# Kernel optimization log

Measured on AMD Instinct MI355X. Metric: run time of the kernel, lower is better.

The kernel has to match this reference:

```python
import jax, jax.numpy as jnp
import numpy as np

SL, BS, D = 2048, 2, 1024
H, DH = 16, 64  # num_heads, nhid

def setup_inputs() -> dict:
    key = jax.random.key(0)
    ks = jax.random.split(key, 8)
    inv = 1.0 / np.sqrt(D)
    return {
        "query": jax.random.normal(ks[0], (SL, BS, D), jnp.float32),
        "keys": jax.random.normal(ks[1], (SL, BS, D), jnp.float32),
        "values": jax.random.normal(ks[2], (SL, BS, D), jnp.float32),
        "mask": jnp.ones((1, 1, SL, SL), jnp.int32),
        "Wq": jax.random.normal(ks[3], (H * DH, D), jnp.float32) * inv,
        "Wk": jax.random.normal(ks[4], (H * DH, D), jnp.float32) * inv,
        "Wv": jax.random.normal(ks[5], (H * DH, D), jnp.float32) * inv,
        "Wo": jax.random.normal(ks[6], (D, H * DH), jnp.float32) * inv,
    }

def reference(query, keys, values, mask, Wq, Wk, Wv, Wo):
    slq, bs, _ = query.shape
    sl = keys.shape[0]
    # nn.Linear(bias=False): x @ W.T ; then view to (s, b, H, DH)
    q = (query @ Wq.T).reshape(slq, bs, H, DH)   # sbhd
    k = (keys @ Wk.T).reshape(sl, bs, H, DH)
    v = (values @ Wv.T).reshape(sl, bs, H, DH)
    # NOTE: original forward never applies self.scale -> unscaled scores.
    scores = jnp.einsum('qbhd,kbhd->bhqk', q, k)
    scores = jnp.where(mask == 0, jnp.float32(-1e20), scores)
    weights = jax.nn.softmax(scores, axis=-1)
    attn = jnp.einsum('bhqk,kbhd->qbhd', weights, v).reshape(slq, bs, H * DH)
    return attn @ Wo.T  # [slq, bs, out_dim]
```

## Files before the change

### kernel.cpp

```cpp
#include <hip/hip_runtime.h>


typedef __attribute__((ext_vector_type(4))) float  f32x4;
typedef __attribute__((ext_vector_type(8))) __bf16 bf16x8;
typedef __attribute__((ext_vector_type(4))) __bf16 bf16x4;

#define SLEN 2048
#define BSZ  2
#define DMODEL 1024
#define NHEAD 16
#define DHEAD 64
#define D2 (2 * DMODEL)

__device__ __forceinline__ void async16(void* lds, const void* g) {
    __builtin_amdgcn_global_load_lds(
        (const __attribute__((address_space(1))) unsigned int*)g,
        (__attribute__((address_space(3))) unsigned int*)lds, 16, 0, 0);
}

__device__ __forceinline__ f32x4 mfma16(bf16x8 a, bf16x8 b, f32x4 c) {
    return __builtin_amdgcn_mfma_f32_16x16x32_bf16(a, b, c, 0, 0, 0);
}

struct CvtArgs {
    const float* src[7];
    __bf16* dst[7];
    int n4[7];
    float scale[7];
    const int* mask;
    unsigned int* flag;
    int maskn4;
};
__global__ void cvt_all(CvtArgs a) {
    const int t = blockIdx.y;
    const int stride = gridDim.x * blockDim.x;
    if (t == 7) {
        bool ok = true;
        for (int i = blockIdx.x * blockDim.x + threadIdx.x; i < a.maskn4; i += stride) {
            int4 v = ((const int4*)a.mask)[i];
            ok = ok && v.x && v.y && v.z && v.w;
        }
        if (!ok) atomicAnd(a.flag, 0u);
        return;
    }
    const float* __restrict__ src = a.src[t];
    __bf16* __restrict__ dst = a.dst[t];
    const int n4 = a.n4[t];
    const float sc = a.scale[t];
    for (int i = blockIdx.x * blockDim.x + threadIdx.x; i < n4; i += stride) {
        float4 v = ((const float4*)src)[i];
        bf16x4 o;
        o[0] = (__bf16)(v.x * sc); o[1] = (__bf16)(v.y * sc);
        o[2] = (__bf16)(v.z * sc); o[3] = (__bf16)(v.w * sc);
        ((bf16x4*)dst)[i] = o;
    }
}

__global__ __launch_bounds__(256, 3) void gemm_qkv(const __bf16* __restrict__ Xq,
                                                   const __bf16* __restrict__ Xk,
                                                   const __bf16* __restrict__ Xv,
                                                   const __bf16* __restrict__ W,
                                                   __bf16* __restrict__ QK,
                                                   __bf16* __restrict__ VT) {
    __shared__ __bf16 At[128 * 64];
    __shared__ __bf16 Bt[128 * 64];
    const int tid = threadIdx.x;
    const int lane = tid & 63, wv = tid >> 6;
    const int l15 = lane & 15, l4 = lane >> 4;
    const int wr = wv >> 1, wc = wv & 1;
    const int srow = lane >> 3;
    const int sbyte = (((lane & 7) ^ srow) << 4);
    const int bm = blockIdx.x, bn = blockIdx.y;
    const __bf16* A = (bn < 8) ? Xq : (bn < 16) ? Xk : Xv;
    const char* Ab = (const char*)(A + (size_t)bm * 128 * DMODEL);
    const char* Bb = (const char*)(W + (size_t)bn * 128 * DMODEL);

    f32x4 acc[4][4];
#pragma unroll
    for (int m = 0; m < 4; m++)
#pragma unroll
        for (int n = 0; n < 4; n++)
#pragma unroll
            for (int r = 0; r < 4; r++) acc[m][n][r] = 0.0f;

    for (int k0 = 0; k0 < DMODEL; k0 += 64) {
        __syncthreads();
#pragma unroll
        for (int i = 0; i < 8; i++) {
            int c = wv * 8 + i;
            if (c < 16) {
                int row = c * 8 + srow;
                async16(&At[c * 512], Ab + ((size_t)row * DMODEL + k0) * 2 + sbyte);
            } else {
                int row = (c - 16) * 8 + srow;
                async16(&Bt[(c - 16) * 512], Bb + ((size_t)row * DMODEL + k0) * 2 + sbyte);
            }
        }
        __syncthreads();

#pragma unroll
        for (int kk = 0; kk < 2; kk++) {
            bf16x8 af[4], bfr[4];
#pragma unroll
            for (int m = 0; m < 4; m++) {
                int row = wr * 64 + m * 16 + l15;
                int col = (kk * 32 + l4 * 8) ^ ((row & 7) << 3);
                af[m] = *(const bf16x8*)&At[row * 64 + col];
            }
#pragma unroll
            for (int n = 0; n < 4; n++) {
                int row = wc * 64 + n * 16 + l15;
                int col = (kk * 32 + l4 * 8) ^ ((row & 7) << 3);
                bfr[n] = *(const bf16x8*)&Bt[row * 64 + col];
            }
#pragma unroll
            for (int m = 0; m < 4; m++)
#pragma unroll
                for (int n = 0; n < 4; n++)
                    acc[m][n] = mfma16(af[m], bfr[n], acc[m][n]);
        }
    }

    if (bn < 16) {
#pragma unroll
        for (int m = 0; m < 4; m++)
#pragma unroll
            for (int n = 0; n < 4; n++)
#pragma unroll
                for (int r = 0; r < 4; r++) {
                    size_t row = (size_t)bm * 128 + wr * 64 + m * 16 + l4 * 4 + r;
                    size_t col = (size_t)bn * 128 + wc * 64 + n * 16 + l15;
                    QK[row * D2 + col] = (__bf16)acc[m][n][r];
                }
    } else {
#pragma unroll
        for (int m = 0; m < 4; m++)
#pragma unroll
            for (int n = 0; n < 4; n++)
#pragma unroll
                for (int r = 0; r < 4; r++) {
                    int t = bm * 128 + wr * 64 + m * 16 + l4 * 4 + r;
                    int hd = (bn - 16) * 128 + wc * 64 + n * 16 + l15;
                    int s = t >> 1, b = t & 1;
                    VT[((size_t)(b * NHEAD * DHEAD + hd)) * SLEN + s] = (__bf16)acc[m][n][r];
                }
    }
}

__global__ __launch_bounds__(256, 2) void gemm_out(const __bf16* __restrict__ A,
                                                   const __bf16* __restrict__ B,
                                                   float* __restrict__ Cv) {
    __shared__ __bf16 At[2][128 * 64];
    __shared__ __bf16 Bt[2][64 * 64];
    const int tid = threadIdx.x;
    const int lane = tid & 63, wv = tid >> 6;
    const int l15 = lane & 15, l4 = lane >> 4;
    const int wr = wv >> 1, wc = wv & 1;
    const int srow = lane >> 3;
    const int sbyte = (((lane & 7) ^ srow) << 4);
    const int bm = blockIdx.x, bn = blockIdx.y;
    const char* Ab = (const char*)(A + (size_t)bm * 128 * DMODEL);
    const char* Bb = (const char*)(B + (size_t)bn * 64 * DMODEL);

    f32x4 acc[4][2];
#pragma unroll
    for (int m = 0; m < 4; m++)
#pragma unroll
        for (int n = 0; n < 2; n++)
#pragma unroll
            for (int r = 0; r < 4; r++) acc[m][n][r] = 0.0f;

    auto stage = [&](int buf, int k0) {
#pragma unroll
        for (int i = 0; i < 6; i++) {
            int c = wv * 6 + i;
            if (c < 16) {
                int row = c * 8 + srow;
                async16(&At[buf][c * 512], Ab + ((size_t)row * DMODEL + k0) * 2 + sbyte);
            } else {
                int row = (c - 16) * 8 + srow;
                async16(&Bt[buf][(c - 16) * 512], Bb + ((size_t)row * DMODEL + k0) * 2 + sbyte);
            }
        }
    };

    stage(0, 0);
    __syncthreads();
    int cur = 0;
    for (int k0 = 0; k0 < DMODEL; k0 += 64) {
        if (k0 + 64 < DMODEL) stage(cur ^ 1, k0 + 64);
#pragma unroll
        for (int kk = 0; kk < 2; kk++) {
            bf16x8 af[4], bfr[2];
#pragma unroll
            for (int m = 0; m < 4; m++) {
                int row = wr * 64 + m * 16 + l15;
                int col = (kk * 32 + l4 * 8) ^ ((row & 7) << 3);
                af[m] = *(const bf16x8*)&At[cur][row * 64 + col];
            }
#pragma unroll
            for (int n = 0; n < 2; n++) {
                int row = wc * 32 + n * 16 + l15;
                int col = (kk * 32 + l4 * 8) ^ ((row & 7) << 3);
                bfr[n] = *(const bf16x8*)&Bt[cur][row * 64 + col];
            }
#pragma unroll
            for (int m = 0; m < 4; m++)
#pragma unroll
                for (int n = 0; n < 2; n++)
                    acc[m][n] = mfma16(af[m], bfr[n], acc[m][n]);
        }
        __syncthreads();
        cur ^= 1;
    }

#pragma unroll
    for (int m = 0; m < 4; m++)
#pragma unroll
        for (int n = 0; n < 2; n++)
#pragma unroll
            for (int r = 0; r < 4; r++) {
                size_t row = (size_t)bm * 128 + wr * 64 + m * 16 + l4 * 4 + r;
                size_t col = (size_t)bn * 64 + wc * 32 + n * 16 + l15;
                Cv[row * DMODEL + col] = acc[m][n][r];
            }
}

__global__ __launch_bounds__(256, 2) void attn_fwd(const __bf16* __restrict__ QK,
                                                   const __bf16* __restrict__ Vt,
                                                   const int* __restrict__ mask,
                                                   const unsigned int* __restrict__ flag,
                                                   __bf16* __restrict__ Attn) {
    __shared__ __bf16 Kt[2][2][64 * 64];
    __shared__ __bf16 Vs[2][2][64 * 64];
    const int tid = threadIdx.x;
    const int lane = tid & 63, wv = tid >> 6;
    const int l15 = lane & 15, l4 = lane >> 4;
    const int blk = blockIdx.x;
    const int xcd = blk & 7, idx = blk >> 3;
    const int bh = xcd + (idx >> 4) * 8;
    const int qt = idx & 15;
    const int b = bh >> 4, h = bh & 15;
    const bool allones = (*flag != 0u);
    const int srow = lane >> 3;
    const int sbyte = (((lane & 7) ^ srow) << 4);

    bf16x8 aq[2][2];
#pragma unroll
    for (int m = 0; m < 2; m++)
#pragma unroll
        for (int kk = 0; kk < 2; kk++) {
            int qrow = qt * 128 + wv * 32 + m * 16 + l15;
            aq[m][kk] = *(const bf16x8*)(QK + ((size_t)(qrow * BSZ + b) * D2 + h * 64 + kk * 32 + l4 * 8));
        }

    bf16x8 ones;
#pragma unroll
    for (int j = 0; j < 8; j++) ones[j] = (__bf16)1.0f;

    f32x4 o[2][4], olr[2];
#pragma unroll
    for (int m = 0; m < 2; m++) {
#pragma unroll
        for (int nd = 0; nd < 4; nd++)
#pragma unroll
            for (int r = 0; r < 4; r++) o[m][nd][r] = 0.0f;
#pragma unroll
        for (int r = 0; r < 4; r++) olr[m][r] = 0.0f;
    }

    const char* Kb = (const char*)QK + ((size_t)b * D2 + DMODEL + h * 64) * 2;
    const char* Vb = (const char*)Vt + ((size_t)bh * 64) * SLEN * 2;

    auto stage = [&](int buf, int kt) {
#pragma unroll
        for (int i = 0; i < 8; i++) {
            int c = wv * 8 + i;
            if (c < 16) {
                int kh = c >> 3, ck = c & 7;
                int p = (ck & 7) * 8 + srow;
                int kperm = (p & 32) + ((p & 12) << 1) + (((p >> 4) & 1) << 2) + (p & 3);
                int krow = kt * 128 + kh * 64 + kperm;
                async16(&Kt[buf][kh][ck * 512],
                        Kb + (size_t)krow * (BSZ * D2 * 2) + sbyte);
            } else {
                int c2 = c - 16;
                int kh = c2 >> 3, ck = c2 & 7;
                int drow = ck * 8 + srow;
                async16(&Vs[buf][kh][ck * 512],
                        Vb + (size_t)drow * (SLEN * 2) + kt * 256 + kh * 128 + sbyte);
            }
        }
    };

    stage(0, 0);
    __syncthreads();
    int cur = 0;

    for (int kt = 0; kt < SLEN / 128; kt++) {
        if (kt + 1 < SLEN / 128) stage(cur ^ 1, kt + 1);

#pragma unroll
        for (int kh = 0; kh < 2; kh++) {
            const __bf16* Kl = Kt[cur][kh];
            const __bf16* Vl = Vs[cur][kh];

            bf16x8 bk[4][2];
#pragma unroll
            for (int n = 0; n < 4; n++) {
                int row = n * 16 + l15;
#pragma unroll
                for (int kk = 0; kk < 2; kk++) {
                    int col = (kk * 32 + l4 * 8) ^ ((row & 7) << 3);
                    bk[n][kk] = *(const bf16x8*)&Kl[row * 64 + col];
                }
            }

            f32x4 s[2][4];
#pragma unroll
            for (int m = 0; m < 2; m++)
#pragma unroll
                for (int n = 0; n < 4; n++)
#pragma unroll
                    for (int r = 0; r < 4; r++) s[m][n][r] = 0.0f;
            __builtin_amdgcn_s_setprio(1);
#pragma unroll
            for (int n = 0; n < 4; n++)
#pragma unroll
                for (int kk = 0; kk < 2; kk++)
#pragma unroll
                    for (int m = 0; m < 2; m++)
                        s[m][n] = mfma16(bk[n][kk], aq[m][kk], s[m][n]);
            __builtin_amdgcn_s_setprio(0);

            if (!allones) {
#pragma unroll
                for (int m = 0; m < 2; m++) {
                    int q = qt * 128 + wv * 32 + m * 16 + l15;
#pragma unroll
                    for (int n = 0; n < 4; n++)
#pragma unroll
                        for (int r = 0; r < 4; r++) {
                            int kg = kt * 128 + kh * 64 + (n >> 1) * 32 + l4 * 8 + (n & 1) * 4 + r;
                            if (mask[(size_t)q * SLEN + kg] == 0) s[m][n][r] = -1e20f;
                        }
                }
            }

            bf16x8 pb8[2][2];
#pragma unroll
            for (int m = 0; m < 2; m++)
#pragma unroll
                for (int half = 0; half < 2; half++)
#pragma unroll
                    for (int nn = 0; nn < 2; nn++)
#pragma unroll
                        for (int r = 0; r < 4; r++) {
                            float p = __builtin_amdgcn_exp2f(s[m][half * 2 + nn][r]);
                            pb8[m][half][nn * 4 + r] = (__bf16)p;
                        }

            __builtin_amdgcn_s_setprio(1);
#pragma unroll
            for (int half = 0; half < 2; half++) {
#pragma unroll
                for (int nd = 0; nd < 4; nd++) {
                    int row = nd * 16 + l15;
                    int col = (half * 32 + l4 * 8) ^ ((row & 7) << 3);
                    bf16x8 av = *(const bf16x8*)&Vl[row * 64 + col];
#pragma unroll
                    for (int m = 0; m < 2; m++)
                        o[m][nd] = mfma16(av, pb8[m][half], o[m][nd]);
                }
#pragma unroll
                for (int m = 0; m < 2; m++)
                    olr[m] = mfma16(ones, pb8[m][half], olr[m]);
            }
            __builtin_amdgcn_s_setprio(0);
        }

        __syncthreads();
        cur ^= 1;
    }

#pragma unroll
    for (int m = 0; m < 2; m++) {
        float inv = 1.0f / olr[m][0];
        int qrow = qt * 128 + wv * 32 + m * 16 + l15;
#pragma unroll
        for (int nd = 0; nd < 4; nd++) {
            bf16x4 ov;
#pragma unroll
            for (int r = 0; r < 4; r++) ov[r] = (__bf16)(o[m][nd][r] * inv);
            *(bf16x4*)(Attn + ((size_t)(qrow * BSZ + b)) * DMODEL + h * 64 + nd * 16 + l4 * 4) = ov;
        }
    }
}

extern "C" void kernel_launch(void* const* d_in, const int* in_sizes, int n_in,
                              void* d_out, int out_size, void* d_ws, size_t ws_size,
                              hipStream_t stream) {
    const float* query  = (const float*)d_in[0];
    const float* keys   = (const float*)d_in[1];
    const float* values = (const float*)d_in[2];
    const int*   mask   = (const int*)d_in[3];
    const float* Wq     = (const float*)d_in[4];
    const float* Wk     = (const float*)d_in[5];
    const float* Wv     = (const float*)d_in[6];
    const float* Wo     = (const float*)d_in[7];
    float* out = (float*)d_out;

    char* ws = (char*)d_ws;
    const size_t MB = 1024 * 1024;
    __bf16* XQ   = (__bf16*)(ws + 0);
    __bf16* XK   = (__bf16*)(ws + 8 * MB);
    __bf16* XV   = (__bf16*)(ws + 16 * MB);
    __bf16* WCAT = (__bf16*)(ws + 24 * MB);
    __bf16* WQB  = WCAT;
    __bf16* WKB  = (__bf16*)(ws + 26 * MB);
    __bf16* WVB  = (__bf16*)(ws + 28 * MB);
    __bf16* WOB  = (__bf16*)(ws + 30 * MB);
    __bf16* QKB  = (__bf16*)(ws + 32 * MB);
    __bf16* VT   = (__bf16*)(ws + 48 * MB);
    __bf16* ATT  = (__bf16*)(ws + 8 * MB);
    unsigned int* flag = (unsigned int*)(ws + 56 * MB);

    (void)hipMemsetAsync(flag, 0xFF, 4, stream);

    const int NTOK = SLEN * BSZ;
    const int NBIG = NTOK * DMODEL / 4, NW = DMODEL * DMODEL / 4;
    const float LOG2E = 1.4426950408889634f;
    CvtArgs ca;
    ca.src[0] = query;  ca.dst[0] = XQ;  ca.n4[0] = NBIG; ca.scale[0] = 1.0f;
    ca.src[1] = keys;   ca.dst[1] = XK;  ca.n4[1] = NBIG; ca.scale[1] = 1.0f;
    ca.src[2] = values; ca.dst[2] = XV;  ca.n4[2] = NBIG; ca.scale[2] = 1.0f;
    ca.src[3] = Wq;     ca.dst[3] = WQB; ca.n4[3] = NW;   ca.scale[3] = LOG2E;
    ca.src[4] = Wk;     ca.dst[4] = WKB; ca.n4[4] = NW;   ca.scale[4] = 1.0f;
    ca.src[5] = Wv;     ca.dst[5] = WVB; ca.n4[5] = NW;   ca.scale[5] = 1.0f;
    ca.src[6] = Wo;     ca.dst[6] = WOB; ca.n4[6] = NW;   ca.scale[6] = 1.0f;
    ca.mask = mask; ca.flag = flag; ca.maskn4 = SLEN * SLEN / 4;
    cvt_all<<<dim3(256, 8), 256, 0, stream>>>(ca);

    gemm_qkv<<<dim3(NTOK / 128, 3 * DMODEL / 128), 256, 0, stream>>>(XQ, XK, XV, WCAT, QKB, VT);

    attn_fwd<<<BSZ * NHEAD * (SLEN / 128), 256, 0, stream>>>(QKB, VT, mask, flag, ATT);

    gemm_out<<<dim3(NTOK / 128, DMODEL / 64), 256, 0, stream>>>(ATT, WOB, out);
}
```

Before: 118.9 us.

## Fuse fp32-to-bf16 activation conversion into QKV GEMM tile loads

Removes the separate conversion pass for the query/keys/values activations. The QKV GEMM now streams fp32 tiles straight into LDS with a swizzled layout and converts to bf16 while building MFMA fragments. This drops a full write and reread of the bf16 activation copies. In exchange, the GEMM moves twice the A-tile bytes per k-step, uses a larger LDS footprint (32KB A tile), and does conversion ALU work in the inner loop, which may reduce occupancy.

```diff
diff --git a/kernel.cpp b/kernel.cpp
--- a/kernel.cpp
+++ b/kernel.cpp
@@ -23,10 +23,10 @@
 }
 
 struct CvtArgs {
-    const float* src[7];
-    __bf16* dst[7];
-    int n4[7];
-    float scale[7];
+    const float* src[4];
+    __bf16* dst[4];
+    int n4[4];
+    float scale[4];
     const int* mask;
     unsigned int* flag;
     int maskn4;
@@ -34,7 +34,7 @@
 __global__ void cvt_all(CvtArgs a) {
     const int t = blockIdx.y;
     const int stride = gridDim.x * blockDim.x;
-    if (t == 7) {
+    if (t == 4) {
         bool ok = true;
         for (int i = blockIdx.x * blockDim.x + threadIdx.x; i < a.maskn4; i += stride) {
             int4 v = ((const int4*)a.mask)[i];
@@ -56,13 +56,13 @@
     }
 }
 
-__global__ __launch_bounds__(256, 3) void gemm_qkv(const __bf16* __restrict__ Xq,
-                                                   const __bf16* __restrict__ Xk,
-                                                   const __bf16* __restrict__ Xv,
+__global__ __launch_bounds__(256, 3) void gemm_qkv(const float* __restrict__ Xq,
+                                                   const float* __restrict__ Xk,
+                                                   const float* __restrict__ Xv,
                                                    const __bf16* __restrict__ W,
                                                    __bf16* __restrict__ QK,
                                                    __bf16* __restrict__ VT) {
-    __shared__ __bf16 At[128 * 64];
+    __shared__ float  Atf[128 * 64];
     __shared__ __bf16 Bt[128 * 64];
     const int tid = threadIdx.x;
     const int lane = tid & 63, wv = tid >> 6;
@@ -71,7 +71,7 @@
     const int srow = lane >> 3;
     const int sbyte = (((lane & 7) ^ srow) << 4);
     const int bm = blockIdx.x, bn = blockIdx.y;
-    const __bf16* A = (bn < 8) ? Xq : (bn < 16) ? Xk : Xv;
+    const float* A = (bn < 8) ? Xq : (bn < 16) ? Xk : Xv;
     const char* Ab = (const char*)(A + (size_t)bm * 128 * DMODEL);
     const char* Bb = (const char*)(W + (size_t)bn * 128 * DMODEL);
 
@@ -86,14 +86,16 @@
     for (int k0 = 0; k0 < DMODEL; k0 += 64) {
         __syncthreads();
 #pragma unroll
-        for (int i = 0; i < 8; i++) {
-            int c = wv * 8 + i;
-            if (c < 16) {
-                int row = c * 8 + srow;
-                async16(&At[c * 512], Ab + ((size_t)row * DMODEL + k0) * 2 + sbyte);
+        for (int i = 0; i < 12; i++) {
+            int c = wv * 12 + i;
+            if (c < 32) {
+                int row = c * 4 + (lane >> 4);
+                int sb = ((lane & 15) << 4) ^ ((row & 7) << 4);
+                async16(&Atf[c * 256], Ab + (size_t)row * (DMODEL * 4) + k0 * 4 + sb);
             } else {
-                int row = (c - 16) * 8 + srow;
-                async16(&Bt[(c - 16) * 512], Bb + ((size_t)row * DMODEL + k0) * 2 + sbyte);
+                int c2 = c - 32;
+                int row = c2 * 8 + srow;
+                async16(&Bt[c2 * 512], Bb + ((size_t)row * DMODEL + k0) * 2 + sbyte);
             }
         }
         __syncthreads();
@@ -104,8 +106,14 @@
 #pragma unroll
             for (int m = 0; m < 4; m++) {
                 int row = wr * 64 + m * 16 + l15;
-                int col = (kk * 32 + l4 * 8) ^ ((row & 7) << 3);
-                af[m] = *(const bf16x8*)&At[row * 64 + col];
+                int basef = kk * 32 + l4 * 8;
+                f32x4 lo = *(const f32x4*)&Atf[row * 64 + (basef ^ ((row & 7) << 2))];
+                f32x4 hi = *(const f32x4*)&Atf[row * 64 + ((basef + 4) ^ ((row & 7) << 2))];
+#pragma unroll
+                for (int j = 0; j < 4; j++) {
+                    af[m][j]     = (__bf16)lo[j];
+                    af[m][4 + j] = (__bf16)hi[j];
+                }
             }
 #pragma unroll
             for (int n = 0; n < 4; n++) {
@@ -412,36 +420,30 @@
 
     char* ws = (char*)d_ws;
     const size_t MB = 1024 * 1024;
-    __bf16* XQ   = (__bf16*)(ws + 0);
-    __bf16* XK   = (__bf16*)(ws + 8 * MB);
-    __bf16* XV   = (__bf16*)(ws + 16 * MB);
-    __bf16* WCAT = (__bf16*)(ws + 24 * MB);
+    __bf16* WCAT = (__bf16*)(ws + 0);
     __bf16* WQB  = WCAT;
-    __bf16* WKB  = (__bf16*)(ws + 26 * MB);
-    __bf16* WVB  = (__bf16*)(ws + 28 * MB);
-    __bf16* WOB  = (__bf16*)(ws + 30 * MB);
-    __bf16* QKB  = (__bf16*)(ws + 32 * MB);
-    __bf16* VT   = (__bf16*)(ws + 48 * MB);
-    __bf16* ATT  = (__bf16*)(ws + 8 * MB);
-    unsigned int* flag = (unsigned int*)(ws + 56 * MB);
+    __bf16* WKB  = (__bf16*)(ws + 2 * MB);
+    __bf16* WVB  = (__bf16*)(ws + 4 * MB);
+    __bf16* WOB  = (__bf16*)(ws + 6 * MB);
+    __bf16* QKB  = (__bf16*)(ws + 8 * MB);
+    __bf16* VT   = (__bf16*)(ws + 24 * MB);
+    __bf16* ATT  = (__bf16*)(ws + 33 * MB);
+    unsigned int* flag = (unsigned int*)(ws + 42 * MB);
 
     (void)hipMemsetAsync(flag, 0xFF, 4, stream);
 
     const int NTOK = SLEN * BSZ;
-    const int NBIG = NTOK * DMODEL / 4, NW = DMODEL * DMODEL / 4;
+    const int NW = DMODEL * DMODEL / 4;
     const float LOG2E = 1.4426950408889634f;
     CvtArgs ca;
-    ca.src[0] = query;  ca.dst[0] = XQ;  ca.n4[0] = NBIG; ca.scale[0] = 1.0f;
-    ca.src[1] = keys;   ca.dst[1] = XK;  ca.n4[1] = NBIG; ca.scale[1] = 1.0f;
-    ca.src[2] = values; ca.dst[2] = XV;  ca.n4[2] = NBIG; ca.scale[2] = 1.0f;
-    ca.src[3] = Wq;     ca.dst[3] = WQB; ca.n4[3] = NW;   ca.scale[3] = LOG2E;
-    ca.src[4] = Wk;     ca.dst[4] = WKB; ca.n4[4] = NW;   ca.scale[4] = 1.0f;
-    ca.src[5] = Wv;     ca.dst[5] = WVB; ca.n4[5] = NW;   ca.scale[5] = 1.0f;
-    ca.src[6] = Wo;     ca.dst[6] = WOB; ca.n4[6] = NW;   ca.scale[6] = 1.0f;
+    ca.src[0] = Wq; ca.dst[0] = WQB; ca.n4[0] = NW; ca.scale[0] = LOG2E;
+    ca.src[1] = Wk; ca.dst[1] = WKB; ca.n4[1] = NW; ca.scale[1] = 1.0f;
+    ca.src[2] = Wv; ca.dst[2] = WVB; ca.n4[2] = NW; ca.scale[2] = 1.0f;
+    ca.src[3] = Wo; ca.dst[3] = WOB; ca.n4[3] = NW; ca.scale[3] = 1.0f;
     ca.mask = mask; ca.flag = flag; ca.maskn4 = SLEN * SLEN / 4;
-    cvt_all<<<dim3(256, 8), 256, 0, stream>>>(ca);
-
-    gemm_qkv<<<dim3(NTOK / 128, 3 * DMODEL / 128), 256, 0, stream>>>(XQ, XK, XV, WCAT, QKB, VT);
+    cvt_all<<<dim3(256, 5), 256, 0, stream>>>(ca);
+
+    gemm_qkv<<<dim3(NTOK / 128, 3 * DMODEL / 128), 256, 0, stream>>>(query, keys, values, WCAT, QKB, VT);
 
     attn_fwd<<<BSZ * NHEAD * (SLEN / 128), 256, 0, stream>>>(QKB, VT, mask, flag, ATT);
 
```

Result: slower. 139.8 us (+17.5%).
